# Kernel optimization log

Hardware: AMD Instinct MI355X
Metric: run time of the kernel (lower is better)

Reference implementation:

```python
import jax, jax.numpy as jnp
import numpy as np

B, S, C = 2, 4096, 640
HEADS = 10
DH = C // HEADS  # 64
SCALE = 1.0 / np.sqrt(DH).astype(np.float32)


def setup_inputs() -> dict:
    key = jax.random.key(0)
    ks = jax.random.split(key, 5)
    w_std = 0.02
    return {
        "hidden_states": jax.random.normal(ks[0], (B, S, C), dtype=jnp.float32),
        "Wq": jax.random.normal(ks[1], (C, C), dtype=jnp.float32) * w_std,
        "Wk": jax.random.normal(ks[2], (C, C), dtype=jnp.float32) * w_std,
        "Wv": jax.random.normal(ks[3], (C, C), dtype=jnp.float32) * w_std,
        "Wo": jax.random.normal(ks[4], (C, C), dtype=jnp.float32) * w_std,
        "b_out": jnp.zeros((C,), dtype=jnp.float32),
    }


def _split_heads(x):
    # [B, S, C] -> [B, H, S, Dh]
    b, s, c = x.shape
    return x.reshape(b, s, HEADS, DH).transpose(0, 2, 1, 3)


def reference(hidden_states, Wq, Wk, Wv, Wo, b_out):
    residual = hidden_states
    # Linear projections (torch nn.Linear: x @ W.T), to_q/k/v have no bias
    q = jnp.einsum("bsc,dc->bsd", hidden_states, Wq)
    k = jnp.einsum("bsc,dc->bsd", hidden_states, Wk)
    v = jnp.einsum("bsc,dc->bsd", hidden_states, Wv)
    q = _split_heads(q)  # [B, H, S, Dh]
    k = _split_heads(k)
    v = _split_heads(v)
    # get_attention_scores: scaled QK^T + softmax (full O(S^2) matrix)
    scores = jnp.einsum("bhqd,bhkd->bhqk", q, k) * SCALE
    probs = jax.nn.softmax(scores, axis=-1)
    out = jnp.einsum("bhqk,bhkd->bhqd", probs, v)  # [B, H, S, Dh]
    # batch_to_head_dim: [B, H, S, Dh] -> [B, S, C]
    out = out.transpose(0, 2, 1, 3).reshape(hidden_states.shape)
    # to_out[0] Linear (with bias), to_out[1] Dropout = identity at eval
    out = jnp.einsum("bsc,dc->bsd", out, Wo) + b_out
    # residual_connection=True, rescale_output_factor=1.0
    return out + residual
```

## Files before the change

kernel.cpp:

```cpp
#include <hip/hip_runtime.h>
#include <stdint.h>
#include <stddef.h>

#define Bsz 2
#define Ssz 4096
#define Csz 640
#define Hn 10
#define Dh 64
#define NSPLIT 2
#define QROWS 81920
#define NITEMS 1280
#define PBLOCKS 1024

typedef __attribute__((ext_vector_type(8))) short bf16x8;
typedef __attribute__((ext_vector_type(4))) float f32x4;
typedef __attribute__((ext_vector_type(16))) float f32x16;
typedef __attribute__((ext_vector_type(2))) unsigned int u32x2;
typedef __attribute__((ext_vector_type(2))) float f32x2;

typedef __attribute__((address_space(1))) void as1_void;
typedef __attribute__((address_space(3))) void as3_void;

__device__ __forceinline__ void async16(const void* g, void* l) {
  __builtin_amdgcn_global_load_lds((as1_void*)(g), (as3_void*)(l), 16, 0, 0);
}

__device__ __forceinline__ ushort f2bf(float f) {
  union { float f; uint32_t u; } v; v.f = f;
  return (ushort)((v.u + 0x7FFFu + ((v.u >> 16) & 1u)) >> 16);
}

__device__ __forceinline__ uint32_t pack_bf16(float lo, float hi) {
  return __builtin_amdgcn_perm(__float_as_uint(hi), __float_as_uint(lo), 0x07060302u);
}

__device__ __forceinline__ float bf_lo(uint32_t u) {
  return __uint_as_float(u << 16);
}
__device__ __forceinline__ float bf_hi(uint32_t u) {
  return __uint_as_float(u & 0xFFFF0000u);
}

__device__ __forceinline__ float fast_exp2(float x) {
#if __has_builtin(__builtin_amdgcn_exp2f)
  return __builtin_amdgcn_exp2f(x);
#else
  return __exp2f(x);
#endif
}

#define QSCALE 0.1803368801111204f

__global__ __launch_bounds__(256) void cvt_all(
    const float* __restrict__ hs, const float* __restrict__ Wq,
    const float* __restrict__ Wk, const float* __restrict__ Wv,
    const float* __restrict__ Wo, ushort* __restrict__ Xbf,
    ushort* __restrict__ Wqb, ushort* __restrict__ Wkb,
    ushort* __restrict__ Wvb, ushort* __restrict__ Wob)
{
  int gb = blockIdx.x;
  const float* in;
  ushort* out;
  int i;
  if (gb < 5120) {
    in = hs; out = Xbf;
    i = gb * 256 + threadIdx.x;
  } else {
    int wj = gb - 5120;
    int mat = wj / 400;
    int rb = wj - mat * 400;
    in  = (mat == 0) ? Wq  : (mat == 1) ? Wk  : (mat == 2) ? Wv  : Wo;
    out = (mat == 0) ? Wqb : (mat == 1) ? Wkb : (mat == 2) ? Wvb : Wob;
    i = rb * 256 + threadIdx.x;
  }
  const float4 v = ((const float4*)in)[i];
  ushort4 o;
  o.x = f2bf(v.x); o.y = f2bf(v.y); o.z = f2bf(v.z); o.w = f2bf(v.w);
  ((ushort4*)out)[i] = o;
}

__global__ __launch_bounds__(256) void gemm_qkv(
    const ushort* __restrict__ A, const ushort* __restrict__ W0,
    const ushort* __restrict__ W1, const ushort* __restrict__ W2,
    ushort* __restrict__ Qh, ushort* __restrict__ Kh, ushort* __restrict__ Vt)
{
  __shared__ ushort SH[128 * 64 * 2];
  ushort* As = SH;
  ushort* Bs = SH + 8192;
  const int t = threadIdx.x;
  const int lane = t & 63;
  const int w = t >> 6;
  const int quad = lane >> 4;
  const int l15 = lane & 15;
  const int m0 = blockIdx.x * 128;
  const int wub = t & ~63;

  const int mat = blockIdx.y / 5;
  const int n0 = (blockIdx.y % 5) * 128;
  const ushort* W = (mat == 0) ? W0 : ((mat == 1) ? W1 : W2);
  const int qm = (w >> 1) * 64;
  const int qn = (w & 1) * 64;

  f32x4 acc[4][4];
  const f32x4 zero4 = {0.f, 0.f, 0.f, 0.f};
#pragma unroll
  for (int i = 0; i < 4; ++i)
#pragma unroll
    for (int j = 0; j < 4; ++j) acc[i][j] = zero4;

  for (int k0 = 0; k0 < Csz; k0 += 64) {
    __syncthreads();
#pragma unroll
    for (int s = 0; s < 4; ++s) {
      int L = s * 256 + t;
      int row = L >> 3, pc = L & 7;
      int c = pc ^ (row & 7);
      async16(A + (size_t)(m0 + row) * Csz + k0 + c * 8,
              (char*)As + (s * 256 + wub) * 16);
    }
#pragma unroll
    for (int s = 0; s < 4; ++s) {
      int L = s * 256 + t;
      int row = L >> 3, pc = L & 7;
      int c = pc ^ (row & 7);
      async16(W + (size_t)(n0 + row) * Csz + k0 + c * 8,
              (char*)Bs + (s * 256 + wub) * 16);
    }
    __syncthreads();
#pragma unroll
    for (int ks = 0; ks < 2; ++ks) {
      bf16x8 af[4], bfr[4];
#pragma unroll
      for (int i = 0; i < 4; ++i) {
        int row = qm + i * 16 + l15;
        int pc = (ks * 4 + quad) ^ (row & 7);
        af[i] = *(const bf16x8*)(As + row * 64 + pc * 8);
      }
#pragma unroll
      for (int j = 0; j < 4; ++j) {
        int row = qn + j * 16 + l15;
        int pc = (ks * 4 + quad) ^ (row & 7);
        bfr[j] = *(const bf16x8*)(Bs + row * 64 + pc * 8);
      }
#pragma unroll
      for (int i = 0; i < 4; ++i)
#pragma unroll
        for (int j = 0; j < 4; ++j)
          acc[i][j] = __builtin_amdgcn_mfma_f32_16x16x32_bf16(af[i], bfr[j], acc[i][j], 0, 0, 0);
    }
  }

  __syncthreads();
  ushort* Tw = SH + w * 4096;
  const int b = m0 >> 12;
  const int sbase = (m0 & 4095) + qm;
  const int rl = lane >> 3;
  const int ck = lane & 7;

  if (mat < 2) {
    const float sc = (mat == 0) ? QSCALE : 1.0f;
#pragma unroll
    for (int j = 0; j < 4; ++j) {
      int nl = j * 16 + l15;
      int cn = nl >> 3, on = nl & 7;
#pragma unroll
      for (int i = 0; i < 4; ++i) {
#pragma unroll
        for (int r = 0; r < 4; ++r) {
          int ml = i * 16 + quad * 4 + r;
          Tw[ml * 64 + (((cn ^ (ml & 7)) << 3) | on)] = f2bf(acc[i][j][r] * sc);
        }
      }
    }
    ushort* __restrict__ dstp = (mat == 0) ? Qh : Kh;
    const int h = (n0 + qn) >> 6;
    const size_t base = ((size_t)(b * Hn + h) * Ssz + sbase) * Dh;
#pragma unroll
    for (int p = 0; p < 8; ++p) {
      int row = p * 8 + rl;
      uint4 vdat = *(const uint4*)(Tw + row * 64 + ((ck ^ (row & 7)) << 3));
      *(uint4*)(dstp + base + (size_t)row * Dh + ck * 8) = vdat;
    }
  } else {
#pragma unroll
    for (int j = 0; j < 4; ++j) {
      int nl = j * 16 + l15;
#pragma unroll
      for (int i = 0; i < 4; ++i) {
        int ml = i * 16 + quad * 4;
        int cm = ml >> 3, om = ml & 7;
        ushort4 pk4;
        pk4.x = f2bf(acc[i][j][0]); pk4.y = f2bf(acc[i][j][1]);
        pk4.z = f2bf(acc[i][j][2]); pk4.w = f2bf(acc[i][j][3]);
        *(ushort4*)(Tw + nl * 64 + (((cm ^ (nl & 7)) << 3) | om)) = pk4;
      }
    }
    const int h = (n0 + qn) >> 6;
    const size_t base = (size_t)(b * Hn + h) * Dh * Ssz + sbase;
#pragma unroll
    for (int p = 0; p < 8; ++p) {
      int row = p * 8 + rl;
      uint4 vdat = *(const uint4*)(Tw + row * 64 + ((ck ^ (row & 7)) << 3));
      *(uint4*)(Vt + base + (size_t)row * Ssz + ck * 8) = vdat;
    }
  }
}

__global__ __launch_bounds__(256) void gemm_out(
    const ushort* __restrict__ Opart, const float* __restrict__ lpart,
    const ushort* __restrict__ W, const float* __restrict__ bias,
    const float* __restrict__ residual, float* __restrict__ outf)
{
  __shared__ ushort As[128 * 64];
  __shared__ ushort Bs[128 * 64];
  const int t = threadIdx.x;
  const int lane = t & 63;
  const int w = t >> 6;
  const int quad = lane >> 4;
  const int l15 = lane & 15;
  const int m0 = blockIdx.x * 128;
  const int wub = t & ~63;
  const int n0 = blockIdx.y * 128;
  const int qm = (w >> 1) * 64;
  const int qn = (w & 1) * 64;

  f32x4 acc[4][4];
  const f32x4 zero4 = {0.f, 0.f, 0.f, 0.f};
#pragma unroll
  for (int i = 0; i < 4; ++i)
#pragma unroll
    for (int j = 0; j < 4; ++j) acc[i][j] = zero4;

  for (int k0 = 0; k0 < Csz; k0 += 64) {
    const int h = k0 >> 6;
    __syncthreads();
#pragma unroll
    for (int s = 0; s < 4; ++s) {
      int L = s * 256 + t;
      int row = L >> 3, pc = L & 7;
      int c = pc ^ (row & 7);
      int m = m0 + row;
      int b = m >> 12, q = m & 4095;
      size_t prow = (size_t)(b * Hn + h) * Ssz + q;
      const ushort* p0 = Opart + prow * 64 + c * 8;
      uint4 v0 = *(const uint4*)(p0);
      uint4 v1 = *(const uint4*)(p0 + (size_t)QROWS * 64);
      float inv = 1.0f / (lpart[prow] + lpart[(size_t)QROWS + prow]);
      uint4 wv;
      wv.x = pack_bf16((bf_lo(v0.x) + bf_lo(v1.x)) * inv,
                       (bf_hi(v0.x) + bf_hi(v1.x)) * inv);
      wv.y = pack_bf16((bf_lo(v0.y) + bf_lo(v1.y)) * inv,
                       (bf_hi(v0.y) + bf_hi(v1.y)) * inv);
      wv.z = pack_bf16((bf_lo(v0.z) + bf_lo(v1.z)) * inv,
                       (bf_hi(v0.z) + bf_hi(v1.z)) * inv);
      wv.w = pack_bf16((bf_lo(v0.w) + bf_lo(v1.w)) * inv,
                       (bf_hi(v0.w) + bf_hi(v1.w)) * inv);
      *(uint4*)((char*)As + (size_t)L * 16) = wv;
    }
#pragma unroll
    for (int s = 0; s < 4; ++s) {
      int L = s * 256 + t;
      int row = L >> 3, pc = L & 7;
      int c = pc ^ (row & 7);
      async16(W + (size_t)(n0 + row) * Csz + k0 + c * 8,
              (char*)Bs + (s * 256 + wub) * 16);
    }
    __syncthreads();
#pragma unroll
    for (int ks = 0; ks < 2; ++ks) {
      bf16x8 af[4], bfr[4];
#pragma unroll
      for (int i = 0; i < 4; ++i) {
        int row = qm + i * 16 + l15;
        int pc = (ks * 4 + quad) ^ (row & 7);
        af[i] = *(const bf16x8*)(As + row * 64 + pc * 8);
      }
#pragma unroll
      for (int j = 0; j < 4; ++j) {
        int row = qn + j * 16 + l15;
        int pc = (ks * 4 + quad) ^ (row & 7);
        bfr[j] = *(const bf16x8*)(Bs + row * 64 + pc * 8);
      }
#pragma unroll
      for (int i = 0; i < 4; ++i)
#pragma unroll
        for (int j = 0; j < 4; ++j)
          acc[i][j] = __builtin_amdgcn_mfma_f32_16x16x32_bf16(af[i], bfr[j], acc[i][j], 0, 0, 0);
    }
  }

#pragma unroll
  for (int j = 0; j < 4; ++j) {
    int n = n0 + qn + j * 16 + l15;
    float bs = bias[n];
#pragma unroll
    for (int i = 0; i < 4; ++i) {
#pragma unroll
      for (int r = 0; r < 4; ++r) {
        int m = m0 + qm + i * 16 + quad * 4 + r;
        size_t idx = (size_t)m * Csz + n;
        outf[idx] = acc[i][j][r] + bs + residual[idx];
      }
    }
  }
}

__global__ __launch_bounds__(256, 4) void attn_k(
    const ushort* __restrict__ Qh, const ushort* __restrict__ Kh,
    const ushort* __restrict__ Vt, ushort* __restrict__ Opart,
    float* __restrict__ lpart)
{
  __shared__ ushort Ks[2][64 * 64];
  __shared__ ushort Vs[2][64 * 64];

  const int t = threadIdx.x;
  const int lane = t & 63;
  const int w = t >> 6;
  const int l31 = lane & 31;
  const int hi = lane >> 5;

  int ka[4];
#pragma unroll
  for (int ks = 0; ks < 4; ++ks)
    ka[ks] = l31 * 128 + (((ks * 2 + hi) ^ (l31 & 7)) << 4);

  const int row8 = lane >> 3;
  const int pcs = lane & 7;

  f32x16 z16;
#pragma unroll
  for (int i = 0; i < 16; ++i) z16[i] = 0.f;

  const char* Kbase = (const char*)&Ks[0][0];
  const char* Vbase = (const char*)&Vs[0][0];

  for (int item = blockIdx.x; item < NITEMS; item += PBLOCKS) {
    const int jj = item >> 3;
    const int x = jj & 31;
    const int team = (item & 7) + ((jj >> 5) << 3);
    const int bh = team % 20;
    const int z = team / 20;

    const size_t qk_off = (size_t)bh * Ssz * Dh;
    const size_t v_off = (size_t)bh * Dh * Ssz;
    const int qbase = x * 128 + w * 32;
    const int kvbase = z * (Ssz / NSPLIT);

    bf16x8 qf[4];
    {
      int q = qbase + l31;
#pragma unroll
      for (int ks = 0; ks < 4; ++ks)
        qf[ks] = *(const bf16x8*)(Qh + qk_off + (size_t)q * Dh + ks * 16 + hi * 8);
    }

    f32x16 Oa[2];
    Oa[0] = z16; Oa[1] = z16;
    f32x2 lp2 = {0.f, 0.f};

#define STAGE(bi, kv)                                                          \
  {                                                                            \
    _Pragma("unroll") for (int s = 0; s < 2; ++s) {                            \
      int i = w * 2 + s;                                                       \
      int row = i * 8 + row8;                                                  \
      int c = pcs ^ (row & 7);                                                 \
      async16(Kh + qk_off + (size_t)(kvbase + (kv) + row) * Dh + c * 8,        \
              (char*)&Ks[bi][0] + i * 1024);                                   \
    }                                                                          \
    _Pragma("unroll") for (int s = 0; s < 2; ++s) {                            \
      int i = w * 2 + s;                                                       \
      int row = i * 8 + row8;                                                  \
      int c = pcs ^ (row & 7);                                                 \
      async16(Vt + v_off + (size_t)row * Ssz + kvbase + (kv) + c * 8,          \
              (char*)&Vs[bi][0] + i * 1024);                                   \
    }                                                                          \
  }

    STAGE(0, 0);

#define ITER(IT, CB, CBO, DO_STAGE)                                            \
  {                                                                            \
    asm volatile("s_barrier" ::: "memory");                                    \
    if (DO_STAGE) {                                                            \
      STAGE((CB) ^ 1, ((IT) + 1) * 64);                                        \
      asm volatile("s_waitcnt vmcnt(4)" ::: "memory");                         \
    } else {                                                                   \
      asm volatile("s_waitcnt vmcnt(0)" ::: "memory");                         \
    }                                                                          \
    asm volatile("s_barrier" ::: "memory");                                    \
    _Pragma("unroll")                                                          \
    for (int tau = 0; tau < 2; ++tau) {                                        \
      f32x16 Sq;                                                               \
      _Pragma("unroll")                                                        \
      for (int ks = 0; ks < 4; ++ks) {                                         \
        bf16x8 kf = *(const bf16x8*)(Kbase + (CBO) + tau * 4096 + ka[ks]);     \
        Sq = __builtin_amdgcn_mfma_f32_32x32x16_bf16(                          \
            kf, qf[ks], ks == 0 ? z16 : Sq, 0, 0, 0);                          \
      }                                                                        \
      uint32_t pk[8];                                                          \
      _Pragma("unroll")                                                        \
      for (int a = 0; a < 8; ++a) {                                            \
        float p0 = fast_exp2(Sq[2 * a]);                                       \
        float p1 = fast_exp2(Sq[2 * a + 1]);                                   \
        f32x2 pp = {p0, p1};                                                   \
        lp2 += pp;                                                             \
        pk[a] = pack_bf16(p0, p1);                                             \
      }                                                                        \
      _Pragma("unroll")                                                        \
      for (int k2 = 0; k2 < 2; ++k2) {                                         \
        const int ks2 = tau * 2 + k2;                                          \
        const int bA = (2 * ks2) & 3;                                          \
        const int bB = (2 * ks2 + 1) & 3;                                      \
        u32x2 r0 = __builtin_amdgcn_permlane32_swap(pk[2 * bA],                \
                                                    pk[2 * bB], false, false); \
        u32x2 r1 = __builtin_amdgcn_permlane32_swap(pk[2 * bA + 1],            \
                                                    pk[2 * bB + 1], false, false); \
        union { uint32_t u[4]; bf16x8 v; } pu;                                 \
        pu.u[0] = r0.x; pu.u[1] = r1.x;                                        \
        pu.u[2] = r0.y; pu.u[3] = r1.y;                                        \
        bf16x8 pf = pu.v;                                                      \
        _Pragma("unroll")                                                      \
        for (int mt = 0; mt < 2; ++mt) {                                       \
          bf16x8 vfr = *(const bf16x8*)(Vbase + (CBO) + mt * 4096 + ka[ks2]);  \
          Oa[mt] = __builtin_amdgcn_mfma_f32_32x32x16_bf16(vfr, pf, Oa[mt],    \
                                                           0, 0, 0);           \
        }                                                                      \
      }                                                                        \
    }                                                                          \
  }

    const int NH = (Ssz / NSPLIT) / 128;
    for (int itp = 0; itp < NH; ++itp) {
      const int it0 = itp * 2;
      ITER(it0, 0, 0, 1);
      ITER(it0 + 1, 1, 8192, (itp + 1 < NH));
    }
#undef ITER
#undef STAGE

    const size_t prow_base = (size_t)z * QROWS + (size_t)bh * Ssz;
    float l_part = lp2.x + lp2.y;
    float l_tot = l_part + __shfl_xor(l_part, 32, 64);
    int q = qbase + l31;
    if (hi == 0) lpart[prow_base + q] = l_tot;
    ushort* dst = Opart + (prow_base + q) * 64;
#pragma unroll
    for (int mt = 0; mt < 2; ++mt) {
#pragma unroll
      for (int gg = 0; gg < 4; ++gg) {
        int dh0 = mt * 32 + 8 * gg + 4 * hi;
        uint2 val;
        val.x = pack_bf16(Oa[mt][4 * gg + 0], Oa[mt][4 * gg + 1]);
        val.y = pack_bf16(Oa[mt][4 * gg + 2], Oa[mt][4 * gg + 3]);
        *(uint2*)(dst + dh0) = val;
      }
    }
  }
}

extern "C" void kernel_launch(void* const* d_in, const int* in_sizes, int n_in,
                              void* d_out, int out_size, void* d_ws, size_t ws_size,
                              hipStream_t stream) {
  (void)in_sizes; (void)n_in; (void)out_size; (void)ws_size;
  const float* hs = (const float*)d_in[0];
  const float* Wq = (const float*)d_in[1];
  const float* Wk = (const float*)d_in[2];
  const float* Wv = (const float*)d_in[3];
  const float* Wo = (const float*)d_in[4];
  const float* bo = (const float*)d_in[5];
  float* out = (float*)d_out;

  char* ws = (char*)d_ws;
  ushort* Xbf = (ushort*)(ws);
  ushort* Wqb = (ushort*)(ws + 10485760);
  ushort* Wkb = (ushort*)(ws + 10485760 + 819200);
  ushort* Wvb = (ushort*)(ws + 10485760 + 2 * 819200);
  ushort* Wob = (ushort*)(ws + 10485760 + 3 * 819200);
  ushort* Qh  = (ushort*)(ws + 13762560);
  ushort* Kh  = (ushort*)(ws + 13762560 + 10485760);
  ushort* Vt  = (ushort*)(ws + 13762560 + 2 * 10485760);
  ushort* Opart = (ushort*)(ws + 55705600);
  float*  lpart = (float*)(ws + 55705600 + 41943040);

  hipLaunchKernelGGL(cvt_all, dim3(6720), dim3(256), 0, stream,
                     hs, Wq, Wk, Wv, Wo, Xbf, Wqb, Wkb, Wvb, Wob);

  hipLaunchKernelGGL(gemm_qkv, dim3(64, 15), dim3(256), 0, stream,
                     Xbf, Wqb, Wkb, Wvb, Qh, Kh, Vt);
  hipLaunchKernelGGL(attn_k, dim3(PBLOCKS), dim3(256), 0, stream,
                     Qh, Kh, Vt, Opart, lpart);
  hipLaunchKernelGGL(gemm_out, dim3(64, 5), dim3(256), 0, stream,
                     Opart, lpart, Wob, bo, hs, out);
}
```

Before: 241.4 us.

## Split split-KV combine into separate kernel and shrink out-projection tiles

Moves the merge of the two split-KV partial outputs and softmax normalization out of the output-projection GEMM into a standalone combine kernel. That kernel writes a normalized bf16 attention tensor in [B,S,C] layout. The GEMM can then load its A tile with async global-to-LDS copies and uses 128x64 tiles over a 64x10 grid, giving more blocks for occupancy. The cost is an extra launch and an extra round trip of the attention output through memory.

```diff
diff --git a/kernel.cpp b/kernel.cpp
--- a/kernel.cpp
+++ b/kernel.cpp
@@ -207,58 +207,42 @@
 }
 
 __global__ __launch_bounds__(256) void gemm_out(
-    const ushort* __restrict__ Opart, const float* __restrict__ lpart,
-    const ushort* __restrict__ W, const float* __restrict__ bias,
-    const float* __restrict__ residual, float* __restrict__ outf)
+    const ushort* __restrict__ A, const ushort* __restrict__ W,
+    const float* __restrict__ bias, const float* __restrict__ residual,
+    float* __restrict__ outf)
 {
   __shared__ ushort As[128 * 64];
-  __shared__ ushort Bs[128 * 64];
+  __shared__ ushort Bs[64 * 64];
   const int t = threadIdx.x;
   const int lane = t & 63;
   const int w = t >> 6;
   const int quad = lane >> 4;
   const int l15 = lane & 15;
   const int m0 = blockIdx.x * 128;
+  const int n0 = blockIdx.y * 64;
   const int wub = t & ~63;
-  const int n0 = blockIdx.y * 128;
   const int qm = (w >> 1) * 64;
-  const int qn = (w & 1) * 64;
-
-  f32x4 acc[4][4];
+  const int qn = (w & 1) * 32;
+
+  f32x4 acc[4][2];
   const f32x4 zero4 = {0.f, 0.f, 0.f, 0.f};
 #pragma unroll
   for (int i = 0; i < 4; ++i)
 #pragma unroll
-    for (int j = 0; j < 4; ++j) acc[i][j] = zero4;
+    for (int j = 0; j < 2; ++j) acc[i][j] = zero4;
 
   for (int k0 = 0; k0 < Csz; k0 += 64) {
-    const int h = k0 >> 6;
     __syncthreads();
 #pragma unroll
     for (int s = 0; s < 4; ++s) {
       int L = s * 256 + t;
       int row = L >> 3, pc = L & 7;
       int c = pc ^ (row & 7);
-      int m = m0 + row;
-      int b = m >> 12, q = m & 4095;
-      size_t prow = (size_t)(b * Hn + h) * Ssz + q;
-      const ushort* p0 = Opart + prow * 64 + c * 8;
-      uint4 v0 = *(const uint4*)(p0);
-      uint4 v1 = *(const uint4*)(p0 + (size_t)QROWS * 64);
-      float inv = 1.0f / (lpart[prow] + lpart[(size_t)QROWS + prow]);
-      uint4 wv;
-      wv.x = pack_bf16((bf_lo(v0.x) + bf_lo(v1.x)) * inv,
-                       (bf_hi(v0.x) + bf_hi(v1.x)) * inv);
-      wv.y = pack_bf16((bf_lo(v0.y) + bf_lo(v1.y)) * inv,
-                       (bf_hi(v0.y) + bf_hi(v1.y)) * inv);
-      wv.z = pack_bf16((bf_lo(v0.z) + bf_lo(v1.z)) * inv,
-                       (bf_hi(v0.z) + bf_hi(v1.z)) * inv);
-      wv.w = pack_bf16((bf_lo(v0.w) + bf_lo(v1.w)) * inv,
-                       (bf_hi(v0.w) + bf_hi(v1.w)) * inv);
-      *(uint4*)((char*)As + (size_t)L * 16) = wv;
-    }
-#pragma unroll
-    for (int s = 0; s < 4; ++s) {
+      async16(A + (size_t)(m0 + row) * Csz + k0 + c * 8,
+              (char*)As + (s * 256 + wub) * 16);
+    }
+#pragma unroll
+    for (int s = 0; s < 2; ++s) {
       int L = s * 256 + t;
       int row = L >> 3, pc = L & 7;
       int c = pc ^ (row & 7);
@@ -268,7 +252,7 @@
     __syncthreads();
 #pragma unroll
     for (int ks = 0; ks < 2; ++ks) {
-      bf16x8 af[4], bfr[4];
+      bf16x8 af[4], bfr[2];
 #pragma unroll
       for (int i = 0; i < 4; ++i) {
         int row = qm + i * 16 + l15;
@@ -276,7 +260,7 @@
         af[i] = *(const bf16x8*)(As + row * 64 + pc * 8);
       }
 #pragma unroll
-      for (int j = 0; j < 4; ++j) {
+      for (int j = 0; j < 2; ++j) {
         int row = qn + j * 16 + l15;
         int pc = (ks * 4 + quad) ^ (row & 7);
         bfr[j] = *(const bf16x8*)(Bs + row * 64 + pc * 8);
@@ -284,13 +268,13 @@
 #pragma unroll
       for (int i = 0; i < 4; ++i)
 #pragma unroll
-        for (int j = 0; j < 4; ++j)
+        for (int j = 0; j < 2; ++j)
           acc[i][j] = __builtin_amdgcn_mfma_f32_16x16x32_bf16(af[i], bfr[j], acc[i][j], 0, 0, 0);
     }
   }
 
 #pragma unroll
-  for (int j = 0; j < 4; ++j) {
+  for (int j = 0; j < 2; ++j) {
     int n = n0 + qn + j * 16 + l15;
     float bs = bias[n];
 #pragma unroll
@@ -458,6 +442,30 @@
   }
 }
 
+__global__ __launch_bounds__(256) void combine_k(
+    const ushort* __restrict__ Opart, const float* __restrict__ lpart,
+    ushort* __restrict__ attnb)
+{
+  int gid = blockIdx.x * 256 + threadIdx.x;
+  int row = gid >> 4;
+  int dh0 = (gid & 15) * 4;
+  int bh = row >> 12, q = row & 4095;
+  int b = bh / Hn, h = bh % Hn;
+  float a0 = 0.f, a1 = 0.f, a2 = 0.f, a3 = 0.f, lsum = 0.f;
+#pragma unroll
+  for (int sp = 0; sp < NSPLIT; ++sp) {
+    uint2 v = *(const uint2*)(Opart + ((size_t)sp * QROWS + row) * 64 + dh0);
+    a0 += bf_lo(v.x); a1 += bf_hi(v.x);
+    a2 += bf_lo(v.y); a3 += bf_hi(v.y);
+    lsum += lpart[(size_t)sp * QROWS + row];
+  }
+  float inv = 1.0f / lsum;
+  uint2 o;
+  o.x = pack_bf16(a0 * inv, a1 * inv);
+  o.y = pack_bf16(a2 * inv, a3 * inv);
+  *(uint2*)(attnb + ((size_t)b * Ssz + q) * Csz + h * Dh + dh0) = o;
+}
+
 extern "C" void kernel_launch(void* const* d_in, const int* in_sizes, int n_in,
                               void* d_out, int out_size, void* d_ws, size_t ws_size,
                               hipStream_t stream) {
@@ -479,6 +487,7 @@
   ushort* Qh  = (ushort*)(ws + 13762560);
   ushort* Kh  = (ushort*)(ws + 13762560 + 10485760);
   ushort* Vt  = (ushort*)(ws + 13762560 + 2 * 10485760);
+  ushort* attnb = (ushort*)(ws + 13762560 + 3 * 10485760);
   ushort* Opart = (ushort*)(ws + 55705600);
   float*  lpart = (float*)(ws + 55705600 + 41943040);
 
@@ -489,6 +498,8 @@
                      Xbf, Wqb, Wkb, Wvb, Qh, Kh, Vt);
   hipLaunchKernelGGL(attn_k, dim3(PBLOCKS), dim3(256), 0, stream,
                      Qh, Kh, Vt, Opart, lpart);
-  hipLaunchKernelGGL(gemm_out, dim3(64, 5), dim3(256), 0, stream,
-                     Opart, lpart, Wob, bo, hs, out);
-}
+  hipLaunchKernelGGL(combine_k, dim3(QROWS / 16), dim3(256), 0, stream,
+                     Opart, lpart, attnb);
+  hipLaunchKernelGGL(gemm_out, dim3(64, 10), dim3(256), 0, stream,
+                     attnb, Wob, bo, hs, out);
+}
```

After: 232.9 us. 3.5% less time.
